# Kernel tuning notes

Hardware: AMD Instinct MI355X
Metric: run time of the kernel (lower is better)

The kernel has to match this reference:

```python
import jax, jax.numpy as jnp
import numpy as np
from jax import lax

DN = ('NCHW', 'OIHW', 'NCHW')

def conv2d(x, w, b, stride):
    y = lax.conv_general_dilated(x, w, (stride, stride), [(1, 1), (1, 1)], dimension_numbers=DN)
    return y + b[None, :, None, None]

def conv_transpose2d(x, w, b):
    # PyTorch ConvTranspose2d(k=3, stride=2, padding=1, output_padding=1)
    # == conv with lhs_dilation=2, pad low = k-1-p = 1, pad high = k-1-p+op = 2,
    # kernel spatially flipped and in/out channel dims swapped.  w: [in, out, kh, kw]
    wf = jnp.flip(w, (2, 3)).transpose(1, 0, 2, 3)  # [out, in, kh, kw]
    y = lax.conv_general_dilated(x, wf, (1, 1), [(1, 2), (1, 2)], lhs_dilation=(2, 2), dimension_numbers=DN)
    return y + b[None, :, None, None]

def setup_inputs() -> dict:
    key = jax.random.key(0)
    ks = jax.random.split(key, 20)
    s = 0.05
    inp = {
        'x':   jax.random.normal(ks[0], (64, 2, 256, 256), jnp.float32),
        'w1':  jax.random.normal(ks[1], (32, 2, 3, 3), jnp.float32) * s,
        'b1':  jnp.zeros((32,), jnp.float32),
        'w2':  jax.random.normal(ks[2], (64, 32, 3, 3), jnp.float32) * s,
        'b2':  jnp.zeros((64,), jnp.float32),
        'w3':  jax.random.normal(ks[3], (128, 64, 3, 3), jnp.float32) * s,
        'b3':  jnp.zeros((128,), jnp.float32),
        'w4':  jax.random.normal(ks[4], (128, 128, 3, 3), jnp.float32) * s,
        'b4':  jnp.zeros((128,), jnp.float32),
        'emb': jax.random.normal(ks[5], (512, 64), jnp.float32) * s,
        'dw1': jax.random.normal(ks[6], (128, 64, 3, 3), jnp.float32) * s,   # ConvTranspose2d weight [in, out, kh, kw]
        'db1': jnp.zeros((64,), jnp.float32),
        'dw2': jax.random.normal(ks[7], (64, 32, 3, 3), jnp.float32) * s,
        'db2': jnp.zeros((32,), jnp.float32),
        'dw3': jax.random.normal(ks[8], (32, 1, 3, 3), jnp.float32) * s,
        'db3': jnp.zeros((1,), jnp.float32),
    }
    return inp

def reference(x, w1, b1, w2, b2, w3, b3, w4, b4, emb, dw1, db1, dw2, db2, dw3, db3):
    # ---- Encoder ----
    h = jax.nn.relu(conv2d(x, w1, b1, 2))
    h = jax.nn.relu(conv2d(h, w2, b2, 2))
    h = jax.nn.relu(conv2d(h, w3, b3, 2))
    encoded = jax.nn.relu(conv2d(h, w4, b4, 1))  # [B, 128, H/8, W/8]

    # ---- VectorQuantizerEMA (inference math: cdist + argmin + lookup, straight-through) ----
    D = emb.shape[1]  # 64
    flat = encoded.reshape(encoded.shape[0], encoded.shape[1], -1).reshape(-1, D)  # [N, 64]
    dist = (jnp.sum(flat * flat, axis=1, keepdims=True)
            - 2.0 * flat @ emb.T
            + jnp.sum(emb * emb, axis=1)[None, :])  # [N, 512]
    idx = jnp.argmin(dist, axis=1)  # [N]
    quantized = emb[idx]            # [N, 64] gather
    q_st = flat + lax.stop_gradient(quantized - flat)  # straight-through estimator
    vq_feature = q_st.reshape(encoded.shape)

    # ---- Decoder ----
    d = jax.nn.relu(conv_transpose2d(vq_feature, dw1, db1))
    d = jax.nn.relu(conv_transpose2d(d, dw2, db2))
    decoded = conv_transpose2d(d, dw3, db3)  # [B, 1, 256, 256]
    return decoded
```

## Files before the change

### kernel.cpp

```cpp
#include <hip/hip_runtime.h>


using short8  = __attribute__((ext_vector_type(8))) short;
using short4v = __attribute__((ext_vector_type(4))) short;
using floatx4 = __attribute__((ext_vector_type(4))) float;

__device__ inline unsigned short bf16rn(float f) {
  unsigned u = __float_as_uint(f);
  unsigned r = (u + 0x7fffu + ((u >> 16) & 1u)) >> 16;
  return (unsigned short)r;
}
__device__ inline float bf2f1(short h) {
  return __uint_as_float(((unsigned)(unsigned short)h) << 16);
}

__device__ const int DKY[9]  = {1, 1, 1, 2, 0, 2, 2, 0, 0};
__device__ const int DKX[9]  = {1, 2, 0, 1, 1, 2, 0, 2, 0};

__global__ __launch_bounds__(256) void ring_zero(short* __restrict__ h,
                                                 short* __restrict__ l,
                                                 int nimg, int PH, int PW, int C) {
  const int RC = (2 * PW + 2 * (PH - 2)) * C;
  int t = blockIdx.x * 256 + threadIdx.x;
  if (t >= nimg * RC) return;
  const int nl = t / RC;
  int rem = t - nl * RC;
  const int p = rem / C;
  const int ch = rem - p * C;
  int r, c;
  if (p < 2 * PW) {
    r = (p < PW) ? 0 : PH - 1;
    c = (p < PW) ? p : p - PW;
  } else {
    int q = p - 2 * PW;
    if (q < PH - 2) { r = 1 + q; c = 0; }
    else { r = 1 + q - (PH - 2); c = PW - 1; }
  }
  const size_t a = (((size_t)nl * PH + r) * PW + c) * C + ch;
  h[a] = 0; l[a] = 0;
}

__global__ __launch_bounds__(256) void ring_zero1(short* __restrict__ h,
                                                  int nimg, int PH, int PW, int C) {
  const int RC = (2 * PW + 2 * (PH - 2)) * C;
  int t = blockIdx.x * 256 + threadIdx.x;
  if (t >= nimg * RC) return;
  const int nl = t / RC;
  int rem = t - nl * RC;
  const int p = rem / C;
  const int ch = rem - p * C;
  int r, c;
  if (p < 2 * PW) {
    r = (p < PW) ? 0 : PH - 1;
    c = (p < PW) ? p : p - PW;
  } else {
    int q = p - 2 * PW;
    if (q < PH - 2) { r = 1 + q; c = 0; }
    else { r = 1 + q - (PH - 2); c = PW - 1; }
  }
  h[(((size_t)nl * PH + r) * PW + c) * C + ch] = 0;
}

__global__ __launch_bounds__(256) void conv1_xt(const float* __restrict__ x,
                                                const float* __restrict__ w,
                                                const float* __restrict__ bias,
                                                short* __restrict__ oh,
                                                short* __restrict__ ol, int NH) {
  int t = blockIdx.x * 256 + threadIdx.x;
  if (t >= NH * 128 * 128) return;
  const int px = t & 16383;
  const int n  = t >> 14;
  const int r = px >> 7, c = px & 127;
  const int ih0 = 2 * r - 1, iw0 = 2 * c - 1;
  float acc[32];
#pragma unroll
  for (int o = 0; o < 32; ++o) acc[o] = bias[o];
  const float* ip = x + (size_t)n * 2 * 65536;
#pragma unroll
  for (int ic = 0; ic < 2; ++ic, ip += 65536) {
    float v[9];
#pragma unroll
    for (int kh = 0; kh < 3; ++kh) {
      const int ih = ih0 + kh;
#pragma unroll
      for (int kw = 0; kw < 3; ++kw) {
        const int iw = iw0 + kw;
        const bool ok = (ih >= 0) && (ih < 256) && (iw < 256) && (iw >= 0);
        v[kh * 3 + kw] = ok ? ip[ih * 256 + iw] : 0.f;
      }
    }
#pragma unroll
    for (int o = 0; o < 32; ++o) {
      float s = acc[o];
#pragma unroll
      for (int k = 0; k < 9; ++k) s = fmaf(v[k], w[(o * 2 + ic) * 9 + k], s);
      acc[o] = s;
    }
  }
  const size_t base = (((size_t)n * 130 + r + 1) * 130 + (c + 1)) * 32;
  short8 vh[4], vl[4];
#pragma unroll
  for (int g = 0; g < 4; ++g) {
#pragma unroll
    for (int kk = 0; kk < 8; ++kk) {
      const float rv = fmaxf(acc[g * 8 + kk], 0.f);
      const unsigned short hh = bf16rn(rv);
      vh[g][kk] = (short)hh;
      vl[g][kk] = (short)bf16rn(rv - __uint_as_float((unsigned)hh << 16));
    }
    *(short8*)(oh + base + g * 8) = vh[g];
    *(short8*)(ol + base + g * 8) = vl[g];
  }
}

template<int CIN, int COUT>
__device__ inline void wprep_conv_body(int t, const float* __restrict__ w,
                                       short* __restrict__ hi,
                                       short* __restrict__ lo) {
  constexpr int MT = COUT / 16;
  const int j = t & 7;
  const int lane = (t >> 3) & 63;
  const int g = t >> 9;
  const int mt = g % MT;
  const int s = g / MT;
  const int icb = s / 9, tap = s - icb * 9;
  const int kh = tap / 3, kw = tap - kh * 3;
  const int m = mt * 16 + (lane & 15);
  const int ic = icb * 32 + ((lane >> 4) << 3) + j;
  const float v = w[((m * CIN + ic) * 3 + kh) * 3 + kw];
  const unsigned short h = bf16rn(v);
  hi[t] = (short)h;
  lo[t] = (short)bf16rn(v - __uint_as_float((unsigned)h << 16));
}

template<int CIN, int COUT>
__device__ inline void wprep_dec_body(int t, const float* __restrict__ w,
                                      short* __restrict__ hi) {
  constexpr int MT = COUT / 16, ICB = CIN / 32;
  const int j = t & 7;
  const int lane = (t >> 3) & 63;
  const int g = t >> 9;
  const int mt = g % MT;
  const int u = g / MT;
  const int icb = u % ICB;
  const int e = u / ICB;
  const int ky = DKY[e], kx = DKX[e];
  const int m = mt * 16 + (lane & 15);
  const int ic = icb * 32 + ((lane >> 4) << 3) + j;
  hi[t] = (short)bf16rn(w[((ic * COUT + m) * 3 + ky) * 3 + kx]);
}

__global__ __launch_bounds__(256) void prep_all(
    const float* __restrict__ w2, const float* __restrict__ w3,
    const float* __restrict__ w4, const float* __restrict__ dw1,
    const float* __restrict__ dw2, const float* __restrict__ emb,
    short* __restrict__ a2h, short* __restrict__ a2l,
    short* __restrict__ a3h, short* __restrict__ a3l,
    short* __restrict__ a4h, short* __restrict__ a4l,
    short* __restrict__ ad1h, short* __restrict__ ad2h,
    float* __restrict__ nrm, short* __restrict__ ebh,
    short* __restrict__ ebl) {
  const int bb = blockIdx.x;
  const int tid = threadIdx.x;
  if (bb < 72) {
    wprep_conv_body<32, 64>(bb * 256 + tid, w2, a2h, a2l);
  } else if (bb < 360) {
    wprep_conv_body<64, 128>((bb - 72) * 256 + tid, w3, a3h, a3l);
  } else if (bb < 936) {
    wprep_conv_body<128, 128>((bb - 360) * 256 + tid, w4, a4h, a4l);
  } else if (bb < 1224) {
    wprep_dec_body<128, 64>((bb - 936) * 256 + tid, dw1, ad1h);
  } else if (bb < 1296) {
    wprep_dec_body<64, 32>((bb - 1224) * 256 + tid, dw2, ad2h);
  } else if (bb < 1424) {
    const int t = (bb - 1296) * 256 + tid;
    const int j  = t & 7;
    const int l  = (t >> 3) & 63;
    const int kk = (t >> 9) & 1;
    const int ct = t >> 10;
    const int code = ct * 16 + (l & 15);
    const int k = kk * 32 + ((l >> 4) << 3) + j;
    const float v = emb[code * 64 + k];
    const unsigned short h = bf16rn(v);
    ebh[t] = (short)h;
    ebl[t] = (short)bf16rn(v - __uint_as_float((unsigned)h << 16));
  } else {
    const int jj = (bb - 1424) * 256 + tid;
    if (jj < 512) {
      float s = 0.f;
      const float* e = emb + jj * 64;
#pragma unroll
      for (int k = 0; k < 64; ++k) s = fmaf(e[k], e[k], s);
      nrm[jj] = s;
    }
  }
}

template<int CIN, int COUT, int OH, int OW, int S, int PHI, int PWI, int PHO, int PWO, int NP>
__global__ __launch_bounds__(256) void conv_mfma_xt(
    const short* __restrict__ xih, const short* __restrict__ xil,
    const short* __restrict__ ah,  const short* __restrict__ al,
    const float* __restrict__ bias,
    short* __restrict__ xoh, short* __restrict__ xol) {
  constexpr int MT = COUT / 16, ICB = CIN / 32;
  constexpr int PXB = 64 * NP, TPB = OH * OW / PXB;
  constexpr int NSL = ICB * 9;
  constexpr int CH  = MT * 64;
  constexpr int CPT = (CH + 255) / 256;
  __shared__ short ash[2][CH * 8];
  __shared__ short asl2[2][CH * 8];
  const int b = blockIdx.x;
  const int n = b / TPB, pt = b % TPB;
  const int tid = threadIdx.x;
  const int lane = tid & 63, wave = tid >> 6;
  const int quad = lane >> 4;
  int rr[NP], cc[NP];
  size_t bbase[NP];
#pragma unroll
  for (int p = 0; p < NP; ++p) {
    const int pl = pt * PXB + wave * (16 * NP) + p * 16 + (lane & 15);
    rr[p] = pl / OW; cc[p] = pl % OW;
    bbase[p] = (((size_t)n * PHI + S * rr[p]) * PWI + S * cc[p]) * CIN + quad * 8;
  }

  floatx4 acc[MT][NP];
#pragma unroll
  for (int mt = 0; mt < MT; ++mt)
#pragma unroll
    for (int p = 0; p < NP; ++p) acc[mt][p] = (floatx4){0.f, 0.f, 0.f, 0.f};

  const short8* __restrict__ ah8 = (const short8*)ah;
  const short8* __restrict__ al8 = (const short8*)al;

  short8 ra[CPT], rl[CPT];
#pragma unroll
  for (int c = 0; c < CPT; ++c) {
    const int idx = tid + c * 256;
    if (idx < CH) { ra[c] = ah8[idx]; rl[c] = al8[idx]; }
  }
#pragma unroll
  for (int c = 0; c < CPT; ++c) {
    const int idx = tid + c * 256;
    if (idx < CH) {
      *(short8*)(ash[0] + idx * 8) = ra[c];
      *(short8*)(asl2[0] + idx * 8) = rl[c];
    }
  }
  __syncthreads();

  int s = 0;
  for (int icb = 0; icb < ICB; ++icb) {
#pragma unroll
    for (int tap = 0; tap < 9; ++tap, ++s) {
      if (s + 1 < NSL) {
        const int base = (s + 1) * CH;
#pragma unroll
        for (int c = 0; c < CPT; ++c) {
          const int idx = tid + c * 256;
          if (idx < CH) { ra[c] = ah8[base + idx]; rl[c] = al8[base + idx]; }
        }
      }
      const int kh = tap / 3, kw = tap - kh * 3;
      short8 bh[NP], bl[NP];
#pragma unroll
      for (int p = 0; p < NP; ++p) {
        const size_t be = bbase[p] + (size_t)(kh * PWI + kw) * CIN + icb * 32;
        bh[p] = *(const short8*)(xih + be);
        bl[p] = *(const short8*)(xil + be);
      }
      const short8* __restrict__ a8h = (const short8*)ash[s & 1];
      const short8* __restrict__ a8l = (const short8*)asl2[s & 1];
#pragma unroll
      for (int mt = 0; mt < MT; ++mt) {
        const short8 wh = a8h[mt * 64 + lane];
        const short8 wl = a8l[mt * 64 + lane];
#pragma unroll
        for (int p = 0; p < NP; ++p) {
          acc[mt][p] = __builtin_amdgcn_mfma_f32_16x16x32_bf16(wh, bh[p], acc[mt][p], 0, 0, 0);
          acc[mt][p] = __builtin_amdgcn_mfma_f32_16x16x32_bf16(wh, bl[p], acc[mt][p], 0, 0, 0);
          acc[mt][p] = __builtin_amdgcn_mfma_f32_16x16x32_bf16(wl, bh[p], acc[mt][p], 0, 0, 0);
        }
      }
      if (s + 1 < NSL) {
        const int nb = (s + 1) & 1;
#pragma unroll
        for (int c = 0; c < CPT; ++c) {
          const int idx = tid + c * 256;
          if (idx < CH) {
            *(short8*)(ash[nb] + idx * 8) = ra[c];
            *(short8*)(asl2[nb] + idx * 8) = rl[c];
          }
        }
        __syncthreads();
      }
    }
  }
#pragma unroll
  for (int p = 0; p < NP; ++p) {
    const size_t ob = (((size_t)n * PHO + rr[p] + 1) * PWO + (cc[p] + 1)) * COUT + quad * 4;
#pragma unroll
    for (int mt = 0; mt < MT; ++mt) {
      short4v sh, sl;
#pragma unroll
      for (int q = 0; q < 4; ++q) {
        const float v = fmaxf(acc[mt][p][q] + bias[mt * 16 + quad * 4 + q], 0.f);
        const unsigned short hh = bf16rn(v);
        sh[q] = (short)hh;
        sl[q] = (short)bf16rn(v - __uint_as_float((unsigned)hh << 16));
      }
      *(short4v*)(xoh + ob + mt * 16) = sh;
      *(short4v*)(xol + ob + mt * 16) = sl;
    }
  }
}

template<int CIN, int COUT, int IH, int IW, int PHI, int PWI, int PHO, int PWO, int NP, int ASTG>
__global__ __launch_bounds__(256) void deconv_bf16_xt(
    const short* __restrict__ xih, const short* __restrict__ ah,
    const float* __restrict__ bias, short* __restrict__ xoh) {
  constexpr int MT = COUT / 16, ICB = CIN / 32;
  constexpr int PXB = 64 * NP, TPB = IH * IW / PXB;
  constexpr int CHI = 9 * MT * 64;
  constexpr int CPT = (CHI + 255) / 256;
  constexpr int PHE[9] = {0, 1, 1, 2, 2, 3, 3, 3, 3};
  constexpr int DE[9]  = {0, 0, 1, 0, 2, 0, 1, 2, 3};
  __shared__ short ash[ASTG ? 2 * CHI * 8 : 1];
  const int b = blockIdx.x;
  const int n = b / TPB, pt = b % TPB;
  const int tid = threadIdx.x;
  const int lane = tid & 63, wave = tid >> 6;
  const int quad = lane >> 4;
  int ii[NP], jj[NP];
  size_t p00[NP];
#pragma unroll
  for (int p = 0; p < NP; ++p) {
    const int pl = pt * PXB + wave * (16 * NP) + p * 16 + (lane & 15);
    ii[p] = pl / IW; jj[p] = pl % IW;
    p00[p] = (((size_t)n * PHI + (ii[p] + 1)) * PWI + (jj[p] + 1)) * CIN + quad * 8;
  }

  floatx4 acc[4][MT][NP];
#pragma unroll
  for (int ph = 0; ph < 4; ++ph)
#pragma unroll
    for (int mt = 0; mt < MT; ++mt)
#pragma unroll
      for (int p = 0; p < NP; ++p) acc[ph][mt][p] = (floatx4){0.f, 0.f, 0.f, 0.f};

  const short8* __restrict__ ah8 = (const short8*)ah;

  short8 ra[ASTG ? CPT : 1];
  if constexpr (ASTG) {
#pragma unroll
    for (int c = 0; c < CPT; ++c) {
      const int idx = tid + c * 256;
      if (idx < CHI) {
        const int e = idx / (MT * 64);
        const int rem = idx - e * (MT * 64);
        ra[c] = ah8[(e * ICB + 0) * (MT * 64) + rem];
      }
    }
#pragma unroll
    for (int c = 0; c < CPT; ++c) {
      const int idx = tid + c * 256;
      if (idx < CHI) *(short8*)(ash + idx * 8) = ra[c];
    }
    __syncthreads();
  }

  for (int icb = 0; icb < ICB; ++icb) {
    short8 bh[NP][4];
#pragma unroll
    for (int p = 0; p < NP; ++p)
#pragma unroll
      for (int d = 0; d < 4; ++d)
        bh[p][d] = *(const short8*)(xih + p00[p] +
                                    (size_t)((d >> 1) * PWI + (d & 1)) * CIN + icb * 32);
    if constexpr (ASTG) {
      if (icb + 1 < ICB) {
#pragma unroll
        for (int c = 0; c < CPT; ++c) {
          const int idx = tid + c * 256;
          if (idx < CHI) {
            const int e = idx / (MT * 64);
            const int rem = idx - e * (MT * 64);
            ra[c] = ah8[(e * ICB + icb + 1) * (MT * 64) + rem];
          }
        }
      }
    }
#pragma unroll
    for (int e = 0; e < 9; ++e) {
      const int ph = PHE[e], d = DE[e];
#pragma unroll
      for (int mt = 0; mt < MT; ++mt) {
        short8 wh;
        if constexpr (ASTG)
          wh = ((const short8*)(ash + (size_t)(icb & 1) * CHI * 8))[(e * MT + mt) * 64 + lane];
        else
          wh = ah8[((e * ICB + icb) * MT + mt) * 64 + lane];
#pragma unroll
        for (int p = 0; p < NP; ++p)
          acc[ph][mt][p] = __builtin_amdgcn_mfma_f32_16x16x32_bf16(
              wh, bh[p][d], acc[ph][mt][p], 0, 0, 0);
      }
    }
    if constexpr (ASTG) {
      if (icb + 1 < ICB) {
        const size_t nb = (size_t)((icb + 1) & 1) * CHI * 8;
#pragma unroll
        for (int c = 0; c < CPT; ++c) {
          const int idx = tid + c * 256;
          if (idx < CHI) *(short8*)(ash + nb + idx * 8) = ra[c];
        }
        __syncthreads();
      }
    }
  }
#pragma unroll
  for (int p = 0; p < NP; ++p)
#pragma unroll
    for (int ph = 0; ph < 4; ++ph) {
      const int oy = 2 * ii[p] + (ph >> 1), ox = 2 * jj[p] + (ph & 1);
      const size_t ob = (((size_t)n * PHO + oy + 1) * PWO + (ox + 1)) * COUT + quad * 4;
#pragma unroll
      for (int mt = 0; mt < MT; ++mt) {
        short4v sh;
#pragma unroll
        for (int q = 0; q < 4; ++q)
          sh[q] = (short)bf16rn(fmaxf(acc[ph][mt][p][q] + bias[mt * 16 + quad * 4 + q], 0.f));
        *(short4v*)(xoh + ob + mt * 16) = sh;
      }
    }
}

__global__ __launch_bounds__(256) void conv4_mfma(
    const short* __restrict__ xthi, const short* __restrict__ xtlo,
    const short* __restrict__ ahi,  const short* __restrict__ alo,
    const float* __restrict__ bias,
    short* __restrict__ ench, short* __restrict__ encl) {
  __shared__ short ash[2][4096];
  __shared__ short asl[2][4096];
  const int b    = blockIdx.x;
  const int n    = b >> 3;
  const int pt   = b & 7;
  const int tid  = threadIdx.x;
  const int lane = tid & 63;
  const int wave = tid >> 6;
  const int kq   = lane >> 4;
  int pl[2];
  size_t bbase[2];
#pragma unroll
  for (int p = 0; p < 2; ++p) {
    pl[p] = pt * 128 + wave * 32 + p * 16 + (lane & 15);
    const int r = pl[p] >> 5, c = pl[p] & 31;
    bbase[p] = (((size_t)n * 34 + r) * 34 + c) * 128 + kq * 8;
  }

  floatx4 acc[8][2];
#pragma unroll
  for (int mt = 0; mt < 8; ++mt)
#pragma unroll
    for (int p = 0; p < 2; ++p) acc[mt][p] = (floatx4){0.f, 0.f, 0.f, 0.f};

  const short8* __restrict__ ah8 = (const short8*)ahi;
  const short8* __restrict__ al8 = (const short8*)alo;

  short8 rah0, rah1, ral0, ral1;
  rah0 = ah8[tid];        rah1 = ah8[tid + 256];
  ral0 = al8[tid];        ral1 = al8[tid + 256];
  *(short8*)(ash[0] + tid * 8) = rah0;
  *(short8*)(ash[0] + (tid + 256) * 8) = rah1;
  *(short8*)(asl[0] + tid * 8) = ral0;
  *(short8*)(asl[0] + (tid + 256) * 8) = ral1;
  __syncthreads();

  int s = 0;
  for (int icb = 0; icb < 4; ++icb) {
#pragma unroll
    for (int tap = 0; tap < 9; ++tap, ++s) {
      if (s < 35) {
        const int nb = (s + 1) * 512;
        rah0 = ah8[nb + tid];        rah1 = ah8[nb + tid + 256];
        ral0 = al8[nb + tid];        ral1 = al8[nb + tid + 256];
      }
      const int kh = tap / 3, kw = tap - kh * 3;
      const short8* __restrict__ a8h = (const short8*)ash[s & 1];
      const short8* __restrict__ a8l = (const short8*)asl[s & 1];
      short8 bh[2], bl[2];
#pragma unroll
      for (int p = 0; p < 2; ++p) {
        const size_t be = bbase[p] + (size_t)(kh * 34 + kw) * 128 + icb * 32;
        bh[p] = *(const short8*)(xthi + be);
        bl[p] = *(const short8*)(xtlo + be);
      }
#pragma unroll
      for (int mt = 0; mt < 8; ++mt) {
        const short8 ah = a8h[mt * 64 + lane];
        const short8 al = a8l[mt * 64 + lane];
#pragma unroll
        for (int p = 0; p < 2; ++p) {
          acc[mt][p] = __builtin_amdgcn_mfma_f32_16x16x32_bf16(ah, bh[p], acc[mt][p], 0, 0, 0);
          acc[mt][p] = __builtin_amdgcn_mfma_f32_16x16x32_bf16(ah, bl[p], acc[mt][p], 0, 0, 0);
          acc[mt][p] = __builtin_amdgcn_mfma_f32_16x16x32_bf16(al, bh[p], acc[mt][p], 0, 0, 0);
        }
      }
      if (s < 35) {
        const int nbuf = (s + 1) & 1;
        *(short8*)(ash[nbuf] + tid * 8) = rah0;
        *(short8*)(ash[nbuf] + (tid + 256) * 8) = rah1;
        *(short8*)(asl[nbuf] + tid * 8) = ral0;
        *(short8*)(asl[nbuf] + (tid + 256) * 8) = ral1;
        __syncthreads();
      }
    }
  }
#pragma unroll
  for (int p = 0; p < 2; ++p) {
    const size_t obase = (size_t)n * 128 * 1024 + pl[p];
#pragma unroll
    for (int mt = 0; mt < 8; ++mt) {
#pragma unroll
      for (int q = 0; q < 4; ++q) {
        const int cout = mt * 16 + kq * 4 + q;
        const float rr = fmaxf(acc[mt][p][q] + bias[cout], 0.f);
        const unsigned short h = bf16rn(rr);
        const size_t oi = obase + (size_t)cout * 1024;
        ench[oi] = (short)h;
        encl[oi] = (short)bf16rn(rr - __uint_as_float((unsigned)h << 16));
      }
    }
  }
}

__global__ __launch_bounds__(256) void vq_mfma(
    const short* __restrict__ fhi, const short* __restrict__ flo,
    const short* __restrict__ ebh, const short* __restrict__ ebl,
    const float* __restrict__ nrm, const float* __restrict__ emb,
    short* __restrict__ d1h) {
  __shared__ int sidx[128];
  const int lane = threadIdx.x & 63;
  const int wave = threadIdx.x >> 6;
  const int n  = blockIdx.x >> 4;
  const int pb = blockIdx.x & 15;

  short8 ah0[2], ah1[2], al0[2], al1[2];
#pragma unroll
  for (int g = 0; g < 2; ++g) {
    const int ch = wave * 32 + g * 16 + (lane & 15);
    const size_t abase = (((size_t)(n * 128 + ch)) * 16 + pb) * 64 + ((lane >> 4) << 3);
    ah0[g] = *(const short8*)(fhi + abase);
    ah1[g] = *(const short8*)(fhi + abase + 32);
    al0[g] = *(const short8*)(flo + abase);
    al1[g] = *(const short8*)(flo + abase + 32);
  }

  float bestv[2][4];
  int   besti[2][4];
#pragma unroll
  for (int g = 0; g < 2; ++g)
#pragma unroll
    for (int q = 0; q < 4; ++q) { bestv[g][q] = 3.4e38f; besti[g][q] = 0; }

  const short8* __restrict__ ebh8 = (const short8*)ebh;
  const short8* __restrict__ ebl8 = (const short8*)ebl;
  for (int ct = 0; ct < 32; ++ct) {
    const int f0 = (ct * 2) * 64 + lane;
    const short8 b0h = ebh8[f0];
    const short8 b1h = ebh8[f0 + 64];
    const short8 b0l = ebl8[f0];
    const short8 b1l = ebl8[f0 + 64];
    const int code = ct * 16 + (lane & 15);
    const float nn = nrm[code];
#pragma unroll
    for (int g = 0; g < 2; ++g) {
      floatx4 acc = {0.f, 0.f, 0.f, 0.f};
      acc = __builtin_amdgcn_mfma_f32_16x16x32_bf16(ah0[g], b0h, acc, 0, 0, 0);
      acc = __builtin_amdgcn_mfma_f32_16x16x32_bf16(ah1[g], b1h, acc, 0, 0, 0);
      acc = __builtin_amdgcn_mfma_f32_16x16x32_bf16(ah0[g], b0l, acc, 0, 0, 0);
      acc = __builtin_amdgcn_mfma_f32_16x16x32_bf16(ah1[g], b1l, acc, 0, 0, 0);
      acc = __builtin_amdgcn_mfma_f32_16x16x32_bf16(al0[g], b0h, acc, 0, 0, 0);
      acc = __builtin_amdgcn_mfma_f32_16x16x32_bf16(al1[g], b1h, acc, 0, 0, 0);
#pragma unroll
      for (int q = 0; q < 4; ++q) {
        const float sc = nn - 2.f * acc[q];
        if (sc < bestv[g][q]) { bestv[g][q] = sc; besti[g][q] = code; }
      }
    }
  }
#pragma unroll
  for (int off = 1; off < 16; off <<= 1) {
#pragma unroll
    for (int g = 0; g < 2; ++g)
#pragma unroll
      for (int q = 0; q < 4; ++q) {
        const float ov = __shfl_xor(bestv[g][q], off, 64);
        const int   oi = __shfl_xor(besti[g][q], off, 64);
        if (ov < bestv[g][q] || (ov == bestv[g][q] && oi < besti[g][q])) {
          bestv[g][q] = ov; besti[g][q] = oi;
        }
      }
  }
  if ((lane & 15) == 0) {
#pragma unroll
    for (int g = 0; g < 2; ++g)
#pragma unroll
      for (int q = 0; q < 4; ++q)
        sidx[wave * 32 + g * 16 + (lane >> 4) * 4 + q] = besti[g][q];
  }
  __syncthreads();
  const int chg = (threadIdx.x & 15) * 8;
  int gi8[8];
#pragma unroll
  for (int k = 0; k < 8; ++k) gi8[k] = sidx[chg + k];
#pragma unroll
  for (int pxg = 0; pxg < 4; ++pxg) {
    const int p = pxg * 16 + (threadIdx.x >> 4);
    const int pix = pb * 64 + p;
    const int r = pix >> 5, c = pix & 31;
    short8 v;
#pragma unroll
    for (int k = 0; k < 8; ++k)
      v[k] = (short)bf16rn(emb[(size_t)gi8[k] * 64 + p]);
    *(short8*)(d1h + (((size_t)n * 34 + r + 1) * 34 + (c + 1)) * 128 + chg) = v;
  }
}

__global__ __launch_bounds__(256) void dec3_xt(const short* __restrict__ xh,
                                               const float* __restrict__ w,
                                               const float* __restrict__ bias,
                                               float* __restrict__ out, int NH) {
  int t = blockIdx.x * 256 + threadIdx.x;
  if (t >= NH * 128 * 128) return;
  const int px = t & 16383;
  const int nl = t >> 14;
  const int i = px >> 7, j = px & 127;
  const float b0 = bias[0];
  float a00 = b0, a01 = b0, a10 = b0, a11 = b0;
  const size_t base00 = (((size_t)nl * 130 + i + 1) * 130 + (j + 1)) * 32;
#pragma unroll
  for (int icg = 0; icg < 4; ++icg) {
    const short8 h00 = *(const short8*)(xh + base00 + icg * 8);
    const short8 h01 = *(const short8*)(xh + base00 + 32 + icg * 8);
    const short8 h10 = *(const short8*)(xh + base00 + 130 * 32 + icg * 8);
    const short8 h11 = *(const short8*)(xh + base00 + 130 * 32 + 32 + icg * 8);
#pragma unroll
    for (int kk = 0; kk < 8; ++kk) {
      const int ic = icg * 8 + kk;
      const float x00 = bf2f1(h00[kk]);
      const float x01 = bf2f1(h01[kk]);
      const float x10 = bf2f1(h10[kk]);
      const float x11 = bf2f1(h11[kk]);
      const float* wp = w + ic * 9;
      a00 = fmaf(x00, wp[4], a00);
      a01 = fmaf(x00, wp[5], fmaf(x01, wp[3], a01));
      a10 = fmaf(x00, wp[7], fmaf(x10, wp[1], a10));
      a11 = fmaf(x00, wp[8], fmaf(x01, wp[6], fmaf(x10, wp[2], fmaf(x11, wp[0], a11))));
    }
  }
  float* op = out + ((size_t)nl * 256 + 2 * i) * 256 + 2 * j;
  op[0] = a00; op[1] = a01; op[256] = a10; op[257] = a11;
}

extern "C" void kernel_launch(void* const* d_in, const int* in_sizes, int n_in,
                              void* d_out, int out_size, void* d_ws, size_t ws_size,
                              hipStream_t stream) {
  const float* x   = (const float*)d_in[0];
  const float* w1  = (const float*)d_in[1];
  const float* b1  = (const float*)d_in[2];
  const float* w2  = (const float*)d_in[3];
  const float* b2  = (const float*)d_in[4];
  const float* w3  = (const float*)d_in[5];
  const float* b3  = (const float*)d_in[6];
  const float* w4  = (const float*)d_in[7];
  const float* b4  = (const float*)d_in[8];
  const float* emb = (const float*)d_in[9];
  const float* dw1 = (const float*)d_in[10];
  const float* db1 = (const float*)d_in[11];
  const float* dw2 = (const float*)d_in[12];
  const float* db2 = (const float*)d_in[13];
  const float* dw3 = (const float*)d_in[14];
  const float* db3 = (const float*)d_in[15];
  float* outp = (float*)d_out;

  const int N = in_sizes[0] / (2 * 256 * 256);
  if (N & 1) return;
  const int NH = N / 2;

  const size_t sx3 = (size_t)N * 66 * 66 * 64;
  const size_t sx2 = (size_t)NH * 130 * 130 * 32;
  const size_t sx4 = (size_t)N * 34 * 34 * 128;
  const size_t se  = (size_t)N * 128 * 1024;
  const size_t sd1 = sx4;
  const size_t smalls = 512 + 18432 + 73728 + 147456 + 73728 + 18432 + 32768;
  const size_t need = (sx3 + sx4 + se + sd1 + smalls) * sizeof(float);
  if (ws_size < need) return;

  float* ws = (float*)d_ws;
  short* x3h = (short*)ws;                 short* x3l = x3h + sx3;
  short* x2h = (short*)(ws + sx3);         short* x2l = x2h + sx2;
  short* x4h = (short*)(ws + sx3);         short* x4l = x4h + sx4;
  short* ech = (short*)(ws + sx3 + sx4);   short* ecl = ech + se;
  short* d1h = (short*)(ws + sx3 + sx4 + se);
  short* d2h = (short*)ws;
  short* d3h = (short*)(ws + sx3);
  float* sm  = ws + sx3 + sx4 + se + sd1;
  float* nrm = sm;
  short* a2h = (short*)(sm + 512);                         short* a2l = a2h + 18432;
  short* a3h = (short*)(sm + 512 + 18432);                 short* a3l = a3h + 73728;
  short* a4h = (short*)(sm + 512 + 18432 + 73728);         short* a4l = a4h + 147456;
  short* ad1h = (short*)(sm + 512 + 18432 + 73728 + 147456);
  short* ad2h = (short*)(sm + 512 + 18432 + 73728 + 147456 + 73728);
  short* ebh = (short*)(sm + 512 + 18432 + 73728 + 147456 + 73728 + 18432); short* ebl = ebh + 32768;

  prep_all<<<1426, 256, 0, stream>>>(w2, w3, w4, dw1, dw2, emb,
                                     a2h, a2l, a3h, a3l, a4h, a4l,
                                     ad1h, ad2h, nrm, ebh, ebl);

  ring_zero<<<(int)((NH * 516 * 32 + 255) / 256), 256, 0, stream>>>(x2h, x2l, NH, 130, 130, 32);
  ring_zero<<<(int)(((size_t)N * 260 * 64 + 255) / 256), 256, 0, stream>>>(x3h, x3l, N, 66, 66, 64);
  for (int half = 0; half < 2; ++half) {
    const int n0 = half * NH;
    conv1_xt<<<NH * 16384 / 256, 256, 0, stream>>>(
        x + (size_t)n0 * 2 * 65536, w1, b1, x2h, x2l, NH);
    conv_mfma_xt<32, 64, 64, 64, 2, 130, 130, 66, 66, 2>
        <<<NH * 32, 256, 0, stream>>>(x2h, x2l, a2h, a2l, b2,
                                      x3h + (size_t)n0 * 66 * 66 * 64,
                                      x3l + (size_t)n0 * 66 * 66 * 64);
  }
  ring_zero<<<(int)(((size_t)N * 132 * 128 + 255) / 256), 256, 0, stream>>>(x4h, x4l, N, 34, 34, 128);
  conv_mfma_xt<64, 128, 32, 32, 2, 66, 66, 34, 34, 2>
      <<<N * 8, 256, 0, stream>>>(x3h, x3l, a3h, a3l, b3, x4h, x4l);
  conv4_mfma<<<N * 8, 256, 0, stream>>>(x4h, x4l, a4h, a4l, b4, ech, ecl);

  ring_zero1<<<(int)(((size_t)N * 132 * 128 + 255) / 256), 256, 0, stream>>>(d1h, N, 34, 34, 128);
  vq_mfma<<<N * 16, 256, 0, stream>>>(ech, ecl, ebh, ebl, nrm, emb, d1h);

  ring_zero1<<<(int)(((size_t)N * 260 * 64 + 255) / 256), 256, 0, stream>>>(d2h, N, 66, 66, 64);
  deconv_bf16_xt<128, 64, 32, 32, 34, 34, 66, 66, 2, 1>
      <<<N * 8, 256, 0, stream>>>(d1h, ad1h, db1, d2h);
  ring_zero1<<<(int)((NH * 516 * 32 + 255) / 256), 256, 0, stream>>>(d3h, NH, 130, 130, 32);
  for (int half = 0; half < 2; ++half) {
    const int n0 = half * NH;
    deconv_bf16_xt<64, 32, 64, 64, 66, 66, 130, 130, 2, 0>
        <<<NH * 32, 256, 0, stream>>>(d2h + (size_t)n0 * 66 * 66 * 64,
                                      ad2h, db2, d3h);
    dec3_xt<<<NH * 16384 / 256, 256, 0, stream>>>(
        d3h, dw3, db3, outp + (size_t)n0 * 65536, NH);
  }
}
```

Baseline: 548.5 us.

## Split conv4 output channels across two waves per pixel tile with 512-thread blocks

Result: slower. 560.8 us (+2.2%).

```diff
diff --git a/kernel.cpp b/kernel.cpp
--- a/kernel.cpp
+++ b/kernel.cpp
@@ -434,7 +434,7 @@
     }
 }
 
-__global__ __launch_bounds__(256) void conv4_mfma(
+__global__ __launch_bounds__(512) void conv4_mfma(
     const short* __restrict__ xthi, const short* __restrict__ xtlo,
     const short* __restrict__ ahi,  const short* __restrict__ alo,
     const float* __restrict__ bias,
@@ -447,32 +447,32 @@
   const int tid  = threadIdx.x;
   const int lane = tid & 63;
   const int wave = tid >> 6;
+  const int pw   = wave >> 1;
+  const int cs   = wave & 1;
   const int kq   = lane >> 4;
   int pl[2];
   size_t bbase[2];
 #pragma unroll
   for (int p = 0; p < 2; ++p) {
-    pl[p] = pt * 128 + wave * 32 + p * 16 + (lane & 15);
+    pl[p] = pt * 128 + pw * 32 + p * 16 + (lane & 15);
     const int r = pl[p] >> 5, c = pl[p] & 31;
     bbase[p] = (((size_t)n * 34 + r) * 34 + c) * 128 + kq * 8;
   }
 
-  floatx4 acc[8][2];
-#pragma unroll
-  for (int mt = 0; mt < 8; ++mt)
+  floatx4 acc[4][2];
+#pragma unroll
+  for (int mt = 0; mt < 4; ++mt)
 #pragma unroll
     for (int p = 0; p < 2; ++p) acc[mt][p] = (floatx4){0.f, 0.f, 0.f, 0.f};
 
   const short8* __restrict__ ah8 = (const short8*)ahi;
   const short8* __restrict__ al8 = (const short8*)alo;
 
-  short8 rah0, rah1, ral0, ral1;
-  rah0 = ah8[tid];        rah1 = ah8[tid + 256];
-  ral0 = al8[tid];        ral1 = al8[tid + 256];
-  *(short8*)(ash[0] + tid * 8) = rah0;
-  *(short8*)(ash[0] + (tid + 256) * 8) = rah1;
-  *(short8*)(asl[0] + tid * 8) = ral0;
-  *(short8*)(asl[0] + (tid + 256) * 8) = ral1;
+  short8 rah, ral;
+  rah = ah8[tid];
+  ral = al8[tid];
+  *(short8*)(ash[0] + tid * 8) = rah;
+  *(short8*)(asl[0] + tid * 8) = ral;
   __syncthreads();
 
   int s = 0;
@@ -481,8 +481,8 @@
     for (int tap = 0; tap < 9; ++tap, ++s) {
       if (s < 35) {
         const int nb = (s + 1) * 512;
-        rah0 = ah8[nb + tid];        rah1 = ah8[nb + tid + 256];
-        ral0 = al8[nb + tid];        ral1 = al8[nb + tid + 256];
+        rah = ah8[nb + tid];
+        ral = al8[nb + tid];
       }
       const int kh = tap / 3, kw = tap - kh * 3;
       const short8* __restrict__ a8h = (const short8*)ash[s & 1];
@@ -495,9 +495,10 @@
         bl[p] = *(const short8*)(xtlo + be);
       }
 #pragma unroll
-      for (int mt = 0; mt < 8; ++mt) {
-        const short8 ah = a8h[mt * 64 + lane];
-        const short8 al = a8l[mt * 64 + lane];
+      for (int mt = 0; mt < 4; ++mt) {
+        const int mtg = cs * 4 + mt;
+        const short8 ah = a8h[mtg * 64 + lane];
+        const short8 al = a8l[mtg * 64 + lane];
 #pragma unroll
         for (int p = 0; p < 2; ++p) {
           acc[mt][p] = __builtin_amdgcn_mfma_f32_16x16x32_bf16(ah, bh[p], acc[mt][p], 0, 0, 0);
@@ -507,10 +508,8 @@
       }
       if (s < 35) {
         const int nbuf = (s + 1) & 1;
-        *(short8*)(ash[nbuf] + tid * 8) = rah0;
-        *(short8*)(ash[nbuf] + (tid + 256) * 8) = rah1;
-        *(short8*)(asl[nbuf] + tid * 8) = ral0;
-        *(short8*)(asl[nbuf] + (tid + 256) * 8) = ral1;
+        *(short8*)(ash[nbuf] + tid * 8) = rah;
+        *(short8*)(asl[nbuf] + tid * 8) = ral;
         __syncthreads();
       }
     }
@@ -519,10 +518,11 @@
   for (int p = 0; p < 2; ++p) {
     const size_t obase = (size_t)n * 128 * 1024 + pl[p];
 #pragma unroll
-    for (int mt = 0; mt < 8; ++mt) {
+    for (int mt = 0; mt < 4; ++mt) {
+      const int mtg = cs * 4 + mt;
 #pragma unroll
       for (int q = 0; q < 4; ++q) {
-        const int cout = mt * 16 + kq * 4 + q;
+        const int cout = mtg * 16 + kq * 4 + q;
         const float rr = fmaxf(acc[mt][p][q] + bias[cout], 0.f);
         const unsigned short h = bf16rn(rr);
         const size_t oi = obase + (size_t)cout * 1024;
@@ -731,7 +731,7 @@
   ring_zero<<<(int)(((size_t)N * 132 * 128 + 255) / 256), 256, 0, stream>>>(x4h, x4l, N, 34, 34, 128);
   conv_mfma_xt<64, 128, 32, 32, 2, 66, 66, 34, 34, 2>
       <<<N * 8, 256, 0, stream>>>(x3h, x3l, a3h, a3l, b3, x4h, x4l);
-  conv4_mfma<<<N * 8, 256, 0, stream>>>(x4h, x4l, a4h, a4l, b4, ech, ecl);
+  conv4_mfma<<<N * 8, 512, 0, stream>>>(x4h, x4l, a4h, a4l, b4, ech, ecl);
 
   ring_zero1<<<(int)(((size_t)N * 132 * 128 + 255) / 256), 256, 0, stream>>>(d1h, N, 34, 34, 128);
   vq_mfma<<<N * 16, 256, 0, stream>>>(ech, ecl, ebh, ebl, nrm, emb, d1h);
```
